# Performance work log

Hardware: AMD Instinct MI355X
Metric: run time of the kernel (lower is better)

The kernel has to match this reference:

```python
import jax, jax.numpy as jnp
import numpy as np

N, F_IN, D_MID, D_HID, H, G, D_TGT = 6144, 128, 128, 64, 4, 12, 16
LEAKY_ALPHA = 0.2
EPS = 1e-9


def setup_inputs() -> dict:
    key = jax.random.key(0)
    ks = jax.random.split(key, 12)
    x = jax.random.normal(ks[0], (N, F_IN), dtype=jnp.float32)
    # 12 graphs of 512 nodes each (sorted segment ids)
    batch = jnp.repeat(jnp.arange(G, dtype=jnp.int32), N // G)
    # counting_attn is block-diagonal per graph with nonnegative random walk counts
    block = (batch[:, None] == batch[None, :]).astype(jnp.float32)
    counting_attn = jax.random.uniform(ks[1], (N, N), dtype=jnp.float32) * block
    s = lambda d: 1.0 / np.sqrt(d).astype(np.float32)
    Wv = jax.random.normal(ks[2], (F_IN, D_MID), jnp.float32) * s(F_IN)
    bv = jnp.zeros((D_MID,), jnp.float32)
    W0 = jax.random.normal(ks[3], (H, D_MID, D_HID), jnp.float32) * s(D_MID)
    al0 = jax.random.normal(ks[4], (H, D_HID), jnp.float32) * s(D_HID)
    ar0 = jax.random.normal(ks[5], (H, D_HID), jnp.float32) * s(D_HID)
    Wf = jax.random.normal(ks[6], (H * D_HID, D_MID), jnp.float32) * s(H * D_HID)
    alf = jax.random.normal(ks[7], (D_MID,), jnp.float32) * s(D_MID)
    arf = jax.random.normal(ks[8], (D_MID,), jnp.float32) * s(D_MID)
    W1 = jax.random.normal(ks[9], (D_MID, D_MID), jnp.float32) * s(D_MID)
    b1 = jnp.zeros((D_MID,), jnp.float32)
    W2 = jax.random.normal(ks[10], (D_MID, D_TGT), jnp.float32) * s(D_MID)
    b2 = jnp.zeros((D_TGT,), jnp.float32)
    return dict(x=x, counting_attn=counting_attn, batch=batch,
                Wv=Wv, bv=bv, W0=W0, al0=al0, ar0=ar0,
                Wf=Wf, alf=alf, arf=arf, W1=W1, b1=b1, W2=W2, b2=b2)


def gwk_head(h, mask, W, al, ar):
    # GWKLayer: elementwise score, LeakyReLU, masked softmax (via max-sub + exp*mask), weighted sum, ELU
    ft = h @ W  # [N, D]
    a1 = jnp.einsum('nd,d->n', ft, al)  # [N]
    a2 = jnp.einsum('nd,d->n', ft, ar)  # [N]
    a = jax.nn.leaky_relu(a1[:, None] + a2[None, :], LEAKY_ALPHA)  # [N, N]
    a = a - jnp.max(a, axis=1, keepdims=True)
    nomi = jnp.exp(a) * mask
    attn = nomi / (jnp.sum(nomi, axis=1, keepdims=True) + EPS)
    return jax.nn.elu(attn @ ft)  # [N, D]


def reference(x, counting_attn, batch, Wv, bv, W0, al0, ar0, Wf, alf, arf, W1, b1, W2, b2):
    # normalize == 'ones' -> no-op; dropout p = 0.0 (eval)
    h = jax.nn.relu(x @ Wv + bv)  # fc_before_gat: [N, D_MID]
    # layer 0: H parallel heads, concatenated along feature dim
    heads = jax.vmap(lambda W, al, ar: gwk_head(h, counting_attn, W, al, ar))(W0, al0, ar0)  # [H, N, D_HID]
    h = jnp.transpose(heads, (1, 0, 2)).reshape(N, H * D_HID)  # [N, 256]
    # final single-head layer back to D_MID
    h = gwk_head(h, counting_attn, Wf, alf, arf)  # [N, D_MID]
    # pooling 'mean' dispatches to global_add_pool (sum per graph) in the source
    pooled = jax.ops.segment_sum(h, batch, num_segments=G)  # [G, D_MID]
    out = jax.nn.relu(pooled @ W1 + b1) @ W2 + b2  # [G, D_TGT]
    return out
```

## Files before the change

kernel.cpp:

```cpp
#include <hip/hip_runtime.h>
#include <math.h>

#define Nn 6144
#define FIN 128
#define DMID 128
#define DHID 64
#define NH 4
#define NG 12
#define NB 512
#define ALPHA 0.2f
#define EPSV 1e-9f

typedef __bf16 bf16x8 __attribute__((ext_vector_type(8)));
typedef float f32x4 __attribute__((ext_vector_type(4)));
typedef unsigned short ushort_t;

union BU { bf16x8 v; uint u[4]; uint4 q; };

__device__ __forceinline__ float leaky(float x){ return x > 0.f ? x : ALPHA*x; }
__device__ __forceinline__ float eluf(float x){ return x > 0.f ? x : __expf(x)-1.f; }
__device__ __forceinline__ uint f2bf(float f){
  uint u = __float_as_uint(f);
  return (u + 0x7FFFu + ((u>>16)&1u)) >> 16;
}
__device__ __forceinline__ float wave_max(float v){
  #pragma unroll
  for (int off=32; off; off>>=1) v = fmaxf(v, __shfl_xor(v, off));
  return v;
}
__device__ __forceinline__ uint4 packW(const float* p, int strd){
  uint4 pk;
  pk.x = f2bf(p[0])      | (f2bf(p[strd])<<16);
  pk.y = f2bf(p[2*strd]) | (f2bf(p[3*strd])<<16);
  pk.z = f2bf(p[4*strd]) | (f2bf(p[5*strd])<<16);
  pk.w = f2bf(p[6*strd]) | (f2bf(p[7*strd])<<16);
  return pk;
}

__global__ __launch_bounds__(256) void k_f1(
    const float* __restrict__ x, const float* __restrict__ Wv, const float* __restrict__ bv,
    const float* __restrict__ W0, const float* __restrict__ al0, const float* __restrict__ ar0,
    ushort_t* __restrict__ ftS, float* __restrict__ a1arr, float* __restrict__ a2arr,
    float* __restrict__ pmax0){
  int b = blockIdx.x; int i0 = b*16;
  int t = threadIdx.x, lane = t&63, w = t>>6;
  int row = lane&15, kg = lane>>4;
  __shared__ ushort_t xs[16][136];
  __shared__ ushort_t hts[16][136];
  __shared__ ushort_t fts[16][264];
  {
    const float* xp = x + (size_t)i0*FIN + t*8;
    float4 f0 = *reinterpret_cast<const float4*>(xp);
    float4 f1 = *reinterpret_cast<const float4*>(xp+4);
    uint4 pk;
    pk.x = f2bf(f0.x)|(f2bf(f0.y)<<16); pk.y = f2bf(f0.z)|(f2bf(f0.w)<<16);
    pk.z = f2bf(f1.x)|(f2bf(f1.y)<<16); pk.w = f2bf(f1.z)|(f2bf(f1.w)<<16);
    *reinterpret_cast<uint4*>(&xs[t>>4][(t&15)*8]) = pk;
  }
  __syncthreads();
  {
    f32x4 acc2[2] = {{0,0,0,0},{0,0,0,0}};
    #pragma unroll
    for (int kt=0; kt<4; ++kt){
      bf16x8 aF = *reinterpret_cast<bf16x8*>(&xs[row][kt*32 + kg*8]);
      #pragma unroll
      for (int e2=0; e2<2; ++e2){
        int nt = w*2+e2;
        BU B;
        B.q = packW(Wv + (size_t)(kt*32 + (lane>>4)*8)*DMID + nt*16 + (lane&15), DMID);
        acc2[e2] = __builtin_amdgcn_mfma_f32_16x16x32_bf16(aF, B.v, acc2[e2], 0, 0, 0);
      }
    }
    #pragma unroll
    for (int e2=0; e2<2; ++e2){
      int nt = w*2+e2;
      float bvv = bv[nt*16+row];
      #pragma unroll
      for (int reg=0; reg<4; ++reg){
        float v = fmaxf(acc2[e2][reg]+bvv, 0.f);
        hts[kg*4+reg][nt*16+row] = (ushort_t)f2bf(v);
      }
    }
  }
  __syncthreads();
  f32x4 acc4[4] = {{0,0,0,0},{0,0,0,0},{0,0,0,0},{0,0,0,0}};
  #pragma unroll
  for (int kt=0; kt<4; ++kt){
    bf16x8 aF = *reinterpret_cast<bf16x8*>(&hts[row][kt*32 + kg*8]);
    #pragma unroll
    for (int nt=0; nt<4; ++nt){
      BU B;
      B.q = packW(W0 + (size_t)w*DMID*DHID + (size_t)(kt*32 + (lane>>4)*8)*DHID
                     + nt*16 + (lane&15), DHID);
      acc4[nt] = __builtin_amdgcn_mfma_f32_16x16x32_bf16(aF, B.v, acc4[nt], 0, 0, 0);
    }
  }
  {
    float alv[4], arv[4];
    #pragma unroll
    for (int nt=0; nt<4; ++nt){ alv[nt] = al0[w*DHID+nt*16+row]; arv[nt] = ar0[w*DHID+nt*16+row]; }
    float s1[4]={0,0,0,0}, s2[4]={0,0,0,0};
    #pragma unroll
    for (int nt=0; nt<4; ++nt)
      #pragma unroll
      for (int reg=0; reg<4; ++reg){
        s1[reg] += acc4[nt][reg]*alv[nt];
        s2[reg] += acc4[nt][reg]*arv[nt];
      }
    #pragma unroll
    for (int off=1; off<16; off<<=1)
      #pragma unroll
      for (int reg=0; reg<4; ++reg){
        s1[reg] += __shfl_xor(s1[reg], off);
        s2[reg] += __shfl_xor(s2[reg], off);
      }
    if (row==0){
      #pragma unroll
      for (int reg=0; reg<4; ++reg){
        a1arr[w*Nn + i0 + kg*4+reg] = s1[reg];
        a2arr[w*Nn + i0 + kg*4+reg] = s2[reg];
      }
    }
    float mm = fmaxf(fmaxf(s2[0],s2[1]), fmaxf(s2[2],s2[3]));
    mm = fmaxf(mm, __shfl_xor(mm,16));
    mm = fmaxf(mm, __shfl_xor(mm,32));
    if (lane==0) pmax0[w*384 + b] = mm;
  }
  #pragma unroll
  for (int nt=0; nt<4; ++nt)
    #pragma unroll
    for (int reg=0; reg<4; ++reg)
      fts[kg*4+reg][w*DHID + nt*16+row] = (ushort_t)f2bf(acc4[nt][reg]);
  __syncthreads();
  {
    int ch = t, hd2 = ch>>6, ct = (ch>>4)&3, c = ch&15;
    int g = b>>5, ktj = (b&31)>>1, half = b&1;
    ushort_t v[16];
    #pragma unroll
    for (int i=0; i<16; ++i) v[i] = fts[i][ch];
    uint4 p0, p1;
    p0.x=(uint)v[0]|((uint)v[1]<<16);  p0.y=(uint)v[2]|((uint)v[3]<<16);
    p0.z=(uint)v[4]|((uint)v[5]<<16);  p0.w=(uint)v[6]|((uint)v[7]<<16);
    p1.x=(uint)v[8]|((uint)v[9]<<16);  p1.y=(uint)v[10]|((uint)v[11]<<16);
    p1.z=(uint)v[12]|((uint)v[13]<<16);p1.w=(uint)v[14]|((uint)v[15]<<16);
    size_t base = (((size_t)(g*4+hd2)*16 + ktj)*4 + ct)*512;
    *reinterpret_cast<uint4*>(ftS + base + ((half*2+0)*16+c)*8) = p0;
    *reinterpret_cast<uint4*>(ftS + base + ((half*2+1)*16+c)*8) = p1;
  }
}

__global__ __launch_bounds__(512) void k_attn0fcf(
    const ushort_t* __restrict__ ftS, const float* __restrict__ a1arr,
    const float* __restrict__ a2arr, const float* __restrict__ pmax0,
    const float* __restrict__ mask, const float* __restrict__ Wf,
    const float* __restrict__ alf, const float* __restrict__ arf,
    ushort_t* __restrict__ ftfS, float* __restrict__ a1f, float* __restrict__ a2f,
    float* __restrict__ pmaxf){
  int b = blockIdx.x;
  int g = b>>5, it = b&31;
  int i0 = g*NB + it*16, jbase = g*NB;
  int t = threadIdx.x, lane = t&63, w = t>>6;
  int hd = w>>1, jh = w&1;
  int row = lane&15, kg = lane>>4;

  __shared__ float aacc[8][4][64][4];
  __shared__ float ad[8][16];
  __shared__ ushort_t h1s[16][264];
  __shared__ ushort_t fts[16][136];
  __shared__ float dpA[8][16], dpB[8][16];

  {
    float mxv = -INFINITY;
    #pragma unroll
    for (int q=0; q<6; ++q) mxv = fmaxf(mxv, pmax0[hd*384 + q*64 + lane]);
    mxv = wave_max(mxv);
    float a1v = a1arr[hd*Nn + i0 + row];
    float mv = leaky(a1v + mxv);
    f32x4 acc[4] = {{0,0,0,0},{0,0,0,0},{0,0,0,0},{0,0,0,0}};
    float dsum = 0.f;
    const float* mrow = mask + (size_t)(i0+row)*Nn;
    size_t fbase = ((size_t)(g*4+hd)*16*4)*512;
    #pragma unroll 2
    for (int c8=0; c8<8; ++c8){
      int kt = jh*8 + c8;
      int jc = jbase + kt*32 + kg*8;
      float4 mk0 = *reinterpret_cast<const float4*>(mrow + jc);
      float4 mk1 = *reinterpret_cast<const float4*>(mrow + jc + 4);
      float4 a20 = *reinterpret_cast<const float4*>(a2arr + hd*Nn + jc);
      float4 a21 = *reinterpret_cast<const float4*>(a2arr + hd*Nn + jc + 4);
      float a2l[8] = {a20.x,a20.y,a20.z,a20.w,a21.x,a21.y,a21.z,a21.w};
      float mkl[8] = {mk0.x,mk0.y,mk0.z,mk0.w,mk1.x,mk1.y,mk1.z,mk1.w};
      float wv[8];
      #pragma unroll
      for (int e=0;e<8;++e){
        float p = __expf(leaky(a1v + a2l[e]) - mv) * mkl[e];
        wv[e] = p; dsum += p;
      }
      BU A;
      #pragma unroll
      for (int q=0;q<4;++q) A.u[q] = f2bf(wv[2*q]) | (f2bf(wv[2*q+1])<<16);
      #pragma unroll
      for (int ct=0; ct<4; ++ct){
        BU B; B.q = *reinterpret_cast<const uint4*>(ftS + fbase + (size_t)(kt*4+ct)*512 + lane*8);
        acc[ct] = __builtin_amdgcn_mfma_f32_16x16x32_bf16(A.v, B.v, acc[ct], 0, 0, 0);
      }
    }
    dsum += __shfl_xor(dsum, 16);
    dsum += __shfl_xor(dsum, 32);
    if (lane < 16) ad[w][lane] = dsum;
    #pragma unroll
    for (int ct=0; ct<4; ++ct)
      *reinterpret_cast<float4*>(&aacc[w][ct][lane][0]) = (float4){acc[ct][0],acc[ct][1],acc[ct][2],acc[ct][3]};
  }
  __syncthreads();
  {
    int w0 = hd*2, w1 = hd*2+1;
    float dr[4];
    #pragma unroll
    for (int reg=0; reg<4; ++reg) dr[reg] = ad[w0][kg*4+reg] + ad[w1][kg*4+reg] + EPSV;
    #pragma unroll
    for (int ci=0; ci<2; ++ci){
      int ct = jh*2+ci;
      float4 A0 = *reinterpret_cast<float4*>(&aacc[w0][ct][lane][0]);
      float4 A1 = *reinterpret_cast<float4*>(&aacc[w1][ct][lane][0]);
      float tot[4] = {A0.x+A1.x, A0.y+A1.y, A0.z+A1.z, A0.w+A1.w};
      #pragma unroll
      for (int reg=0; reg<4; ++reg){
        float o = eluf(tot[reg]/dr[reg]);
        h1s[kg*4+reg][hd*64 + ct*16 + row] = (ushort_t)f2bf(o);
      }
    }
  }
  __syncthreads();
  {
    f32x4 acc2 = {0,0,0,0};
    #pragma unroll
    for (int kt=0; kt<8; ++kt){
      bf16x8 aF = *reinterpret_cast<bf16x8*>(&h1s[row][kt*32 + kg*8]);
      BU B;
      B.q = packW(Wf + (size_t)(kt*32 + (lane>>4)*8)*DMID + w*16 + (lane&15), DMID);
      acc2 = __builtin_amdgcn_mfma_f32_16x16x32_bf16(aF, B.v, acc2, 0, 0, 0);
    }
    float alv = alf[w*16+row], arv = arf[w*16+row];
    float s1[4], s2[4];
    #pragma unroll
    for (int reg=0; reg<4; ++reg){
      s1[reg] = acc2[reg]*alv;
      s2[reg] = acc2[reg]*arv;
      fts[kg*4+reg][w*16+row] = (ushort_t)f2bf(acc2[reg]);
    }
    #pragma unroll
    for (int off=1; off<16; off<<=1)
      #pragma unroll
      for (int reg=0; reg<4; ++reg){
        s1[reg] += __shfl_xor(s1[reg], off);
        s2[reg] += __shfl_xor(s2[reg], off);
      }
    if (row==0){
      #pragma unroll
      for (int reg=0; reg<4; ++reg){ dpA[w][kg*4+reg]=s1[reg]; dpB[w][kg*4+reg]=s2[reg]; }
    }
  }
  __syncthreads();
  if (t < 16){
    float v1=0.f, v2=0.f;
    #pragma unroll
    for (int q=0; q<8; ++q){ v1 += dpA[q][t]; v2 += dpB[q][t]; }
    a1f[i0+t] = v1; a2f[i0+t] = v2;
    float m = v2;
    #pragma unroll
    for (int off=1; off<16; off<<=1) m = fmaxf(m, __shfl_xor(m, off));
    if (t==0) pmaxf[b] = m;
  }
  if (t < 256){
    int ch = t>>1, half8 = t&1;
    int ct = ch>>4, c = ch&15;
    int gg = b>>5, ktj = (b&31)>>1, half = b&1;
    ushort_t v[8];
    #pragma unroll
    for (int i=0; i<8; ++i) v[i] = fts[half8*8+i][ch];
    uint4 pk;
    pk.x=(uint)v[0]|((uint)v[1]<<16); pk.y=(uint)v[2]|((uint)v[3]<<16);
    pk.z=(uint)v[4]|((uint)v[5]<<16); pk.w=(uint)v[6]|((uint)v[7]<<16);
    int kslot = half*2 + half8;
    size_t base = ((size_t)(gg*16+ktj)*8 + ct)*512;
    *reinterpret_cast<uint4*>(ftfS + base + (kslot*16+c)*8) = pk;
  }
}

__global__ __launch_bounds__(256) void k_attnf(
    const ushort_t* __restrict__ ftfS, const float* __restrict__ a1f,
    const float* __restrict__ a2f, const float* __restrict__ pmaxf,
    const float* __restrict__ mask, float* __restrict__ ppart){
  int b = blockIdx.x;
  int g = b>>5, it = b&31;
  int i0 = g*NB + it*16, jbase = g*NB;
  int t = threadIdx.x, lane = t&63, w = t>>6;
  int row = lane&15, kg = lane>>4;
  __shared__ float s_acc[4][8][64][4];
  __shared__ float s_d[4][16];
  float mxv = -INFINITY;
  #pragma unroll
  for (int q=0; q<6; ++q) mxv = fmaxf(mxv, pmaxf[q*64 + lane]);
  mxv = wave_max(mxv);
  float a1v = a1f[i0+row];
  float mv = leaky(a1v + mxv);
  f32x4 acc[8];
  #pragma unroll
  for (int ct=0; ct<8; ++ct) acc[ct] = (f32x4){0,0,0,0};
  float dsum = 0.f;
  const float* mrow = mask + (size_t)(i0+row)*Nn;
  #pragma unroll 2
  for (int c4=0; c4<4; ++c4){
    int kt = w*4 + c4;
    int jc = jbase + kt*32 + kg*8;
    float4 mk0 = *reinterpret_cast<const float4*>(mrow + jc);
    float4 mk1 = *reinterpret_cast<const float4*>(mrow + jc + 4);
    float4 a20 = *reinterpret_cast<const float4*>(a2f + jc);
    float4 a21 = *reinterpret_cast<const float4*>(a2f + jc + 4);
    float a2l[8] = {a20.x,a20.y,a20.z,a20.w,a21.x,a21.y,a21.z,a21.w};
    float mkl[8] = {mk0.x,mk0.y,mk0.z,mk0.w,mk1.x,mk1.y,mk1.z,mk1.w};
    float wv[8];
    #pragma unroll
    for (int e=0;e<8;++e){
      float p = __expf(leaky(a1v + a2l[e]) - mv) * mkl[e];
      wv[e] = p; dsum += p;
    }
    BU A;
    #pragma unroll
    for (int q=0;q<4;++q) A.u[q] = f2bf(wv[2*q]) | (f2bf(wv[2*q+1])<<16);
    #pragma unroll
    for (int ct=0; ct<8; ++ct){
      BU B; B.q = *reinterpret_cast<const uint4*>(ftfS + ((size_t)(g*16+kt)*8 + ct)*512 + lane*8);
      acc[ct] = __builtin_amdgcn_mfma_f32_16x16x32_bf16(A.v, B.v, acc[ct], 0, 0, 0);
    }
  }
  dsum += __shfl_xor(dsum, 16);
  dsum += __shfl_xor(dsum, 32);
  if (lane < 16) s_d[w][lane] = dsum;
  #pragma unroll
  for (int ct=0; ct<8; ++ct)
    *reinterpret_cast<float4*>(&s_acc[w][ct][lane][0]) = (float4){acc[ct][0],acc[ct][1],acc[ct][2],acc[ct][3]};
  __syncthreads();
  float dr[4];
  #pragma unroll
  for (int reg=0; reg<4; ++reg)
    dr[reg] = s_d[0][kg*4+reg] + s_d[1][kg*4+reg] + s_d[2][kg*4+reg] + s_d[3][kg*4+reg] + EPSV;
  #pragma unroll
  for (int ci=0; ci<2; ++ci){
    int ct = w*2 + ci;
    float4 A0 = *reinterpret_cast<float4*>(&s_acc[0][ct][lane][0]);
    float4 A1 = *reinterpret_cast<float4*>(&s_acc[1][ct][lane][0]);
    float4 A2 = *reinterpret_cast<float4*>(&s_acc[2][ct][lane][0]);
    float4 A3 = *reinterpret_cast<float4*>(&s_acc[3][ct][lane][0]);
    float tot[4] = {A0.x+A1.x+A2.x+A3.x, A0.y+A1.y+A2.y+A3.y,
                    A0.z+A1.z+A2.z+A3.z, A0.w+A1.w+A2.w+A3.w};
    float psum = 0.f;
    #pragma unroll
    for (int reg=0; reg<4; ++reg) psum += eluf(tot[reg]/dr[reg]);
    psum += __shfl_xor(psum, 16);
    psum += __shfl_xor(psum, 32);
    if (lane < 16) ppart[(size_t)b*DMID + ct*16 + lane] = psum;
  }
}

__global__ __launch_bounds__(256) void k_mlp(
    const float* __restrict__ ppart, const float* __restrict__ W1, const float* __restrict__ b1,
    const float* __restrict__ W2, const float* __restrict__ b2, float* __restrict__ out){
  int g = blockIdx.x;
  int t = threadIdx.x;
  __shared__ float red[8][DMID];
  __shared__ float ps[DMID], ts[DMID];
  __shared__ float p2[2][DMID];
  __shared__ float p4[2][16];
  {
    float4 s4 = {0,0,0,0};
    #pragma unroll
    for (int gi=0; gi<4; ++gi){
      int itx = (t>>5) + gi*8;
      float4 v = *reinterpret_cast<const float4*>(ppart + (size_t)(g*32+itx)*DMID + (t&31)*4);
      s4.x += v.x; s4.y += v.y; s4.z += v.z; s4.w += v.w;
    }
    *reinterpret_cast<float4*>(&red[t>>5][(t&31)*4]) = s4;
  }
  __syncthreads();
  if (t < DMID){
    float s = 0.f;
    #pragma unroll
    for (int q=0; q<8; ++q) s += red[q][t];
    ps[t] = s;
  }
  __syncthreads();
  {
    int col = t & 127, half = t>>7;
    float acc = 0.f;
    #pragma unroll 8
    for (int k=half*64; k<half*64+64; ++k) acc += ps[k]*W1[k*DMID+col];
    p2[half][col] = acc;
  }
  __syncthreads();
  if (t < DMID) ts[t] = fmaxf(p2[0][t]+p2[1][t]+b1[t], 0.f);
  __syncthreads();
  if (t < 32){
    int col = t & 15, half = t>>4;
    float acc = 0.f;
    #pragma unroll 8
    for (int k=half*64; k<half*64+64; ++k) acc += ts[k]*W2[k*16+col];
    p4[half][col] = acc;
  }
  __syncthreads();
  if (t < 16) out[g*16+t] = p4[0][t]+p4[1][t]+b2[t];
}

extern "C" void kernel_launch(void* const* d_in, const int* in_sizes, int n_in,
                              void* d_out, int out_size, void* d_ws, size_t ws_size,
                              hipStream_t stream) {
  const float* x    = (const float*)d_in[0];
  const float* mask = (const float*)d_in[1];
  const float* Wv   = (const float*)d_in[3];
  const float* bv   = (const float*)d_in[4];
  const float* W0   = (const float*)d_in[5];
  const float* al0  = (const float*)d_in[6];
  const float* ar0  = (const float*)d_in[7];
  const float* Wf   = (const float*)d_in[8];
  const float* alf  = (const float*)d_in[9];
  const float* arf  = (const float*)d_in[10];
  const float* W1   = (const float*)d_in[11];
  const float* b1   = (const float*)d_in[12];
  const float* W2   = (const float*)d_in[13];
  const float* b2   = (const float*)d_in[14];
  float* out = (float*)d_out;

  char* W = (char*)d_ws;
  ushort_t* ftS  = (ushort_t*)(W);
  ushort_t* ftfS = (ushort_t*)(W + 3145728);
  float* a1arr = (float*)(W + 4718592);
  float* a2arr = (float*)(W + 4816896);
  float* a1f   = (float*)(W + 4915200);
  float* a2f   = (float*)(W + 4939776);
  float* pmax0 = (float*)(W + 4964352);
  float* pmaxf = (float*)(W + 4970496);
  float* ppart = (float*)(W + 4972032);

  hipLaunchKernelGGL(k_f1,       dim3(Nn/16), dim3(256), 0, stream,
                     x, Wv, bv, W0, al0, ar0, ftS, a1arr, a2arr, pmax0);
  hipLaunchKernelGGL(k_attn0fcf, dim3(NG*32), dim3(512), 0, stream,
                     ftS, a1arr, a2arr, pmax0, mask, Wf, alf, arf, ftfS, a1f, a2f, pmaxf);
  hipLaunchKernelGGL(k_attnf,    dim3(NG*32), dim3(256), 0, stream,
                     ftfS, a1f, a2f, pmaxf, mask, ppart);
  hipLaunchKernelGGL(k_mlp,      dim3(NG),    dim3(256), 0, stream,
                     ppart, W1, b1, W2, b2, out);
}
```

Baseline: 55.69 us.

## Fuse pooling MLP into final attention kernel via last-block atomic counter

Drops the separate MLP kernel launch: each attention block writes its partial pooled sums and bumps a per-graph atomic counter, and the last block per graph runs the reduction and the two-layer MLP. The counter is reset in the first kernel. The row-max read now takes only the 32 partial maxima belonging to the current graph instead of all of them, which changes the softmax shift but not the normalized result. Loop unroll factors are also raised. The last-block pattern relies on threadfence ordering and serializes the MLP tail onto one block per graph.

```diff
diff --git a/kernel.cpp b/kernel.cpp
--- a/kernel.cpp
+++ b/kernel.cpp
@@ -41,10 +41,11 @@
     const float* __restrict__ x, const float* __restrict__ Wv, const float* __restrict__ bv,
     const float* __restrict__ W0, const float* __restrict__ al0, const float* __restrict__ ar0,
     ushort_t* __restrict__ ftS, float* __restrict__ a1arr, float* __restrict__ a2arr,
-    float* __restrict__ pmax0){
+    float* __restrict__ pmax0, int* __restrict__ cnt){
   int b = blockIdx.x; int i0 = b*16;
   int t = threadIdx.x, lane = t&63, w = t>>6;
   int row = lane&15, kg = lane>>4;
+  if (b == 0 && t < NG) cnt[t] = 0;
   __shared__ ushort_t xs[16][136];
   __shared__ ushort_t hts[16][136];
   __shared__ ushort_t fts[16][264];
@@ -170,17 +171,15 @@
   __shared__ float dpA[8][16], dpB[8][16];
 
   {
-    float mxv = -INFINITY;
-    #pragma unroll
-    for (int q=0; q<6; ++q) mxv = fmaxf(mxv, pmax0[hd*384 + q*64 + lane]);
-    mxv = wave_max(mxv);
+    float pm = (lane < 32) ? pmax0[hd*384 + g*32 + lane] : -INFINITY;
+    float mxv = wave_max(pm);
     float a1v = a1arr[hd*Nn + i0 + row];
     float mv = leaky(a1v + mxv);
     f32x4 acc[4] = {{0,0,0,0},{0,0,0,0},{0,0,0,0},{0,0,0,0}};
     float dsum = 0.f;
     const float* mrow = mask + (size_t)(i0+row)*Nn;
     size_t fbase = ((size_t)(g*4+hd)*16*4)*512;
-    #pragma unroll 2
+    #pragma unroll 4
     for (int c8=0; c8<8; ++c8){
       int kt = jh*8 + c8;
       int jc = jbase + kt*32 + kg*8;
@@ -291,7 +290,10 @@
 __global__ __launch_bounds__(256) void k_attnf(
     const ushort_t* __restrict__ ftfS, const float* __restrict__ a1f,
     const float* __restrict__ a2f, const float* __restrict__ pmaxf,
-    const float* __restrict__ mask, float* __restrict__ ppart){
+    const float* __restrict__ mask,
+    const float* __restrict__ W1, const float* __restrict__ b1,
+    const float* __restrict__ W2, const float* __restrict__ b2,
+    float* __restrict__ ppart, int* __restrict__ cnt, float* __restrict__ out){
   int b = blockIdx.x;
   int g = b>>5, it = b&31;
   int i0 = g*NB + it*16, jbase = g*NB;
@@ -299,117 +301,114 @@
   int row = lane&15, kg = lane>>4;
   __shared__ float s_acc[4][8][64][4];
   __shared__ float s_d[4][16];
-  float mxv = -INFINITY;
-  #pragma unroll
-  for (int q=0; q<6; ++q) mxv = fmaxf(mxv, pmaxf[q*64 + lane]);
-  mxv = wave_max(mxv);
-  float a1v = a1f[i0+row];
-  float mv = leaky(a1v + mxv);
-  f32x4 acc[8];
-  #pragma unroll
-  for (int ct=0; ct<8; ++ct) acc[ct] = (f32x4){0,0,0,0};
-  float dsum = 0.f;
-  const float* mrow = mask + (size_t)(i0+row)*Nn;
-  #pragma unroll 2
-  for (int c4=0; c4<4; ++c4){
-    int kt = w*4 + c4;
-    int jc = jbase + kt*32 + kg*8;
-    float4 mk0 = *reinterpret_cast<const float4*>(mrow + jc);
-    float4 mk1 = *reinterpret_cast<const float4*>(mrow + jc + 4);
-    float4 a20 = *reinterpret_cast<const float4*>(a2f + jc);
-    float4 a21 = *reinterpret_cast<const float4*>(a2f + jc + 4);
-    float a2l[8] = {a20.x,a20.y,a20.z,a20.w,a21.x,a21.y,a21.z,a21.w};
-    float mkl[8] = {mk0.x,mk0.y,mk0.z,mk0.w,mk1.x,mk1.y,mk1.z,mk1.w};
-    float wv[8];
-    #pragma unroll
-    for (int e=0;e<8;++e){
-      float p = __expf(leaky(a1v + a2l[e]) - mv) * mkl[e];
-      wv[e] = p; dsum += p;
-    }
-    BU A;
-    #pragma unroll
-    for (int q=0;q<4;++q) A.u[q] = f2bf(wv[2*q]) | (f2bf(wv[2*q+1])<<16);
-    #pragma unroll
-    for (int ct=0; ct<8; ++ct){
-      BU B; B.q = *reinterpret_cast<const uint4*>(ftfS + ((size_t)(g*16+kt)*8 + ct)*512 + lane*8);
-      acc[ct] = __builtin_amdgcn_mfma_f32_16x16x32_bf16(A.v, B.v, acc[ct], 0, 0, 0);
-    }
-  }
-  dsum += __shfl_xor(dsum, 16);
-  dsum += __shfl_xor(dsum, 32);
-  if (lane < 16) s_d[w][lane] = dsum;
-  #pragma unroll
-  for (int ct=0; ct<8; ++ct)
-    *reinterpret_cast<float4*>(&s_acc[w][ct][lane][0]) = (float4){acc[ct][0],acc[ct][1],acc[ct][2],acc[ct][3]};
-  __syncthreads();
-  float dr[4];
-  #pragma unroll
-  for (int reg=0; reg<4; ++reg)
-    dr[reg] = s_d[0][kg*4+reg] + s_d[1][kg*4+reg] + s_d[2][kg*4+reg] + s_d[3][kg*4+reg] + EPSV;
-  #pragma unroll
-  for (int ci=0; ci<2; ++ci){
-    int ct = w*2 + ci;
-    float4 A0 = *reinterpret_cast<float4*>(&s_acc[0][ct][lane][0]);
-    float4 A1 = *reinterpret_cast<float4*>(&s_acc[1][ct][lane][0]);
-    float4 A2 = *reinterpret_cast<float4*>(&s_acc[2][ct][lane][0]);
-    float4 A3 = *reinterpret_cast<float4*>(&s_acc[3][ct][lane][0]);
-    float tot[4] = {A0.x+A1.x+A2.x+A3.x, A0.y+A1.y+A2.y+A3.y,
-                    A0.z+A1.z+A2.z+A3.z, A0.w+A1.w+A2.w+A3.w};
-    float psum = 0.f;
-    #pragma unroll
-    for (int reg=0; reg<4; ++reg) psum += eluf(tot[reg]/dr[reg]);
-    psum += __shfl_xor(psum, 16);
-    psum += __shfl_xor(psum, 32);
-    if (lane < 16) ppart[(size_t)b*DMID + ct*16 + lane] = psum;
-  }
-}
-
-__global__ __launch_bounds__(256) void k_mlp(
-    const float* __restrict__ ppart, const float* __restrict__ W1, const float* __restrict__ b1,
-    const float* __restrict__ W2, const float* __restrict__ b2, float* __restrict__ out){
-  int g = blockIdx.x;
-  int t = threadIdx.x;
-  __shared__ float red[8][DMID];
+  __shared__ float red[2][DMID];
   __shared__ float ps[DMID], ts[DMID];
-  __shared__ float p2[2][DMID];
   __shared__ float p4[2][16];
-  {
-    float4 s4 = {0,0,0,0};
-    #pragma unroll
-    for (int gi=0; gi<4; ++gi){
-      int itx = (t>>5) + gi*8;
-      float4 v = *reinterpret_cast<const float4*>(ppart + (size_t)(g*32+itx)*DMID + (t&31)*4);
-      s4.x += v.x; s4.y += v.y; s4.z += v.z; s4.w += v.w;
-    }
-    *reinterpret_cast<float4*>(&red[t>>5][(t&31)*4]) = s4;
-  }
-  __syncthreads();
-  if (t < DMID){
-    float s = 0.f;
-    #pragma unroll
-    for (int q=0; q<8; ++q) s += red[q][t];
-    ps[t] = s;
-  }
-  __syncthreads();
-  {
-    int col = t & 127, half = t>>7;
-    float acc = 0.f;
-    #pragma unroll 8
-    for (int k=half*64; k<half*64+64; ++k) acc += ps[k]*W1[k*DMID+col];
-    p2[half][col] = acc;
-  }
-  __syncthreads();
-  if (t < DMID) ts[t] = fmaxf(p2[0][t]+p2[1][t]+b1[t], 0.f);
-  __syncthreads();
-  if (t < 32){
-    int col = t & 15, half = t>>4;
-    float acc = 0.f;
-    #pragma unroll 8
-    for (int k=half*64; k<half*64+64; ++k) acc += ts[k]*W2[k*16+col];
-    p4[half][col] = acc;
-  }
-  __syncthreads();
-  if (t < 16) out[g*16+t] = p4[0][t]+p4[1][t]+b2[t];
+  __shared__ int flag;
+  {
+    float pm = (lane < 32) ? pmaxf[g*32 + lane] : -INFINITY;
+    float mxv = wave_max(pm);
+    float a1v = a1f[i0+row];
+    float mv = leaky(a1v + mxv);
+    f32x4 acc[8];
+    #pragma unroll
+    for (int ct=0; ct<8; ++ct) acc[ct] = (f32x4){0,0,0,0};
+    float dsum = 0.f;
+    const float* mrow = mask + (size_t)(i0+row)*Nn;
+    #pragma unroll
+    for (int c4=0; c4<4; ++c4){
+      int kt = w*4 + c4;
+      int jc = jbase + kt*32 + kg*8;
+      float4 mk0 = *reinterpret_cast<const float4*>(mrow + jc);
+      float4 mk1 = *reinterpret_cast<const float4*>(mrow + jc + 4);
+      float4 a20 = *reinterpret_cast<const float4*>(a2f + jc);
+      float4 a21 = *reinterpret_cast<const float4*>(a2f + jc + 4);
+      float a2l[8] = {a20.x,a20.y,a20.z,a20.w,a21.x,a21.y,a21.z,a21.w};
+      float mkl[8] = {mk0.x,mk0.y,mk0.z,mk0.w,mk1.x,mk1.y,mk1.z,mk1.w};
+      float wv[8];
+      #pragma unroll
+      for (int e=0;e<8;++e){
+        float p = __expf(leaky(a1v + a2l[e]) - mv) * mkl[e];
+        wv[e] = p; dsum += p;
+      }
+      BU A;
+      #pragma unroll
+      for (int q=0;q<4;++q) A.u[q] = f2bf(wv[2*q]) | (f2bf(wv[2*q+1])<<16);
+      #pragma unroll
+      for (int ct=0; ct<8; ++ct){
+        BU B; B.q = *reinterpret_cast<const uint4*>(ftfS + ((size_t)(g*16+kt)*8 + ct)*512 + lane*8);
+        acc[ct] = __builtin_amdgcn_mfma_f32_16x16x32_bf16(A.v, B.v, acc[ct], 0, 0, 0);
+      }
+    }
+    dsum += __shfl_xor(dsum, 16);
+    dsum += __shfl_xor(dsum, 32);
+    if (lane < 16) s_d[w][lane] = dsum;
+    #pragma unroll
+    for (int ct=0; ct<8; ++ct)
+      *reinterpret_cast<float4*>(&s_acc[w][ct][lane][0]) = (float4){acc[ct][0],acc[ct][1],acc[ct][2],acc[ct][3]};
+  }
+  __syncthreads();
+  {
+    float dr[4];
+    #pragma unroll
+    for (int reg=0; reg<4; ++reg)
+      dr[reg] = s_d[0][kg*4+reg] + s_d[1][kg*4+reg] + s_d[2][kg*4+reg] + s_d[3][kg*4+reg] + EPSV;
+    #pragma unroll
+    for (int ci=0; ci<2; ++ci){
+      int ct = w*2 + ci;
+      float4 A0 = *reinterpret_cast<float4*>(&s_acc[0][ct][lane][0]);
+      float4 A1 = *reinterpret_cast<float4*>(&s_acc[1][ct][lane][0]);
+      float4 A2 = *reinterpret_cast<float4*>(&s_acc[2][ct][lane][0]);
+      float4 A3 = *reinterpret_cast<float4*>(&s_acc[3][ct][lane][0]);
+      float tot[4] = {A0.x+A1.x+A2.x+A3.x, A0.y+A1.y+A2.y+A3.y,
+                      A0.z+A1.z+A2.z+A3.z, A0.w+A1.w+A2.w+A3.w};
+      float psum = 0.f;
+      #pragma unroll
+      for (int reg=0; reg<4; ++reg) psum += eluf(tot[reg]/dr[reg]);
+      psum += __shfl_xor(psum, 16);
+      psum += __shfl_xor(psum, 32);
+      if (lane < 16) ppart[(size_t)b*DMID + ct*16 + lane] = psum;
+    }
+  }
+  __threadfence();
+  __syncthreads();
+  if (t == 0){
+    int old = atomicAdd(&cnt[g], 1);
+    flag = (old == 31) ? 1 : 0;
+  }
+  __syncthreads();
+  if (flag){
+    __threadfence();
+    {
+      int part = t>>7, col = t&127;
+      float s = 0.f;
+      #pragma unroll
+      for (int q=0; q<16; ++q) s += ppart[(size_t)(g*32 + part*16 + q)*DMID + col];
+      red[part][col] = s;
+    }
+    __syncthreads();
+    if (t < DMID) ps[t] = red[0][t] + red[1][t];
+    __syncthreads();
+    {
+      int col = t&127, half = t>>7;
+      float accv = 0.f;
+      #pragma unroll 8
+      for (int k=half*64; k<half*64+64; ++k) accv += ps[k]*W1[k*DMID+col];
+      red[half][col] = accv;
+    }
+    __syncthreads();
+    if (t < DMID) ts[t] = fmaxf(red[0][t] + red[1][t] + b1[t], 0.f);
+    __syncthreads();
+    if (t < 32){
+      int col = t&15, half = t>>4;
+      float accv = 0.f;
+      #pragma unroll 8
+      for (int k=half*64; k<half*64+64; ++k) accv += ts[k]*W2[k*16+col];
+      p4[half][col] = accv;
+    }
+    __syncthreads();
+    if (t < 16) out[g*16+t] = p4[0][t] + p4[1][t] + b2[t];
+  }
 }
 
 extern "C" void kernel_launch(void* const* d_in, const int* in_sizes, int n_in,
@@ -441,13 +440,12 @@
   float* pmax0 = (float*)(W + 4964352);
   float* pmaxf = (float*)(W + 4970496);
   float* ppart = (float*)(W + 4972032);
+  int*   cnt   = (int*)  (W + 5168640);
 
   hipLaunchKernelGGL(k_f1,       dim3(Nn/16), dim3(256), 0, stream,
-                     x, Wv, bv, W0, al0, ar0, ftS, a1arr, a2arr, pmax0);
+                     x, Wv, bv, W0, al0, ar0, ftS, a1arr, a2arr, pmax0, cnt);
   hipLaunchKernelGGL(k_attn0fcf, dim3(NG*32), dim3(512), 0, stream,
                      ftS, a1arr, a2arr, pmax0, mask, Wf, alf, arf, ftfS, a1f, a2f, pmaxf);
   hipLaunchKernelGGL(k_attnf,    dim3(NG*32), dim3(256), 0, stream,
-                     ftfS, a1f, a2f, pmaxf, mask, ppart);
-  hipLaunchKernelGGL(k_mlp,      dim3(NG),    dim3(256), 0, stream,
-                     ppart, W1, b1, W2, b2, out);
-}
+                     ftfS, a1f, a2f, pmaxf, mask, W1, b1, W2, b2, ppart, cnt, out);
+}
```

Result: slower. 79.21 us (+42.2%).
